# Performance work log

Hardware: AMD Instinct MI355X
Metric: run time of the kernel (lower is better)

Reference implementation:

```python
import jax, jax.numpy as jnp
import numpy as np

N, E, F_IN, H = 50000, 800000, 500, 96

def setup_inputs() -> dict:
    key = jax.random.key(0)
    ks = jax.random.split(key, 10)
    x = jax.random.normal(ks[0], (N, F_IN), dtype=jnp.float32)
    src = jax.random.randint(ks[1], (E,), 0, N, dtype=jnp.int32)
    dst = jax.random.randint(ks[2], (E,), 0, N, dtype=jnp.int32)
    perm = jax.random.permutation(ks[3], N).astype(jnp.int32)
    W1 = jax.random.normal(ks[4], (F_IN, H), dtype=jnp.float32) / np.sqrt(F_IN)
    b1 = jnp.zeros((H,), jnp.float32)
    a1 = jnp.full((H,), 0.25, jnp.float32)  # PReLU init
    W2 = jax.random.normal(ks[5], (H, H), dtype=jnp.float32) / np.sqrt(H)
    b2 = jnp.zeros((H,), jnp.float32)
    a2 = jnp.full((H,), 0.25, jnp.float32)
    Wm = jax.random.normal(ks[6], (H, H), dtype=jnp.float32) / np.sqrt(H)
    bm = jnp.zeros((H,), jnp.float32)
    return {"x": x, "src": src, "dst": dst, "perm": perm,
            "W1": W1, "b1": b1, "a1": a1, "W2": W2, "b2": b2, "a2": a2,
            "Wm": Wm, "bm": bm}

def reference(x, src, dst, perm, W1, b1, a1, W2, b2, a2, Wm, bm):
    n = x.shape[0]
    ones = jnp.ones_like(src, dtype=x.dtype)
    deg_out = jnp.clip(jax.ops.segment_sum(ones, src, num_segments=n), 1.0)
    deg_in = jnp.clip(jax.ops.segment_sum(ones, dst, num_segments=n), 1.0)
    norm_out = (deg_out ** -0.5)[:, None]  # [N,1]
    norm_in = (deg_in ** -0.5)[:, None]

    def gconv(h, W, b, a):
        # DGL GraphConv, norm='both': D_out^-1/2 -> W -> A -> D_in^-1/2 -> +b -> PReLU
        h = (h * norm_out) @ W                                  # [N,H]
        agg = jax.ops.segment_sum(h[src], dst, num_segments=n)  # SpMM via gather/scatter
        h = agg * norm_in + b
        return jnp.where(h >= 0, h, a * h)                      # PReLU

    def encode(feat):
        h = gconv(feat, W1, b1, a1)
        return gconv(h, W2, b2, a2)

    z1 = encode(x)
    z2 = encode(x[perm])  # corrupted view: permuted node features
    z1 = z1 @ Wm + bm
    z2 = z2 @ Wm + bm
    return jnp.concatenate([z1.sum(1), z2.sum(1)], axis=0)  # [2N]
```

## Files before the change

kernel.cpp:

```cpp
#include <hip/hip_runtime.h>

#define H96 96

typedef __attribute__((ext_vector_type(8))) short bf16x8_t;
typedef __attribute__((ext_vector_type(4))) float f32x4_t;
typedef __attribute__((ext_vector_type(8))) _Float16 half8_t;

__global__ void deg_kernel(const int* __restrict__ src, const int* __restrict__ dst,
                           int* __restrict__ dout, int* __restrict__ din, int E) {
    int e = blockIdx.x * blockDim.x + threadIdx.x;
    if (e < E) {
        atomicAdd(dout + src[e], 1);
        atomicAdd(din + dst[e], 1);
    }
}

__global__ void norm_kernel(const int* __restrict__ dO, const int* __restrict__ dI,
                            float* __restrict__ no, float* __restrict__ ni, int N) {
    int i = blockIdx.x * blockDim.x + threadIdx.x;
    if (i < N) {
        no[i] = rsqrtf(fmaxf((float)dO[i], 1.0f));
        ni[i] = rsqrtf(fmaxf((float)dI[i], 1.0f));
    }
}

__global__ void scanA_kernel(const int* __restrict__ in, int* __restrict__ pre,
                             int* __restrict__ bsums, int n) {
    __shared__ int s[256];
    int i = blockIdx.x * 256 + threadIdx.x;
    int v = (i < n) ? in[i] : 0;
    s[threadIdx.x] = v;
    __syncthreads();
    for (int off = 1; off < 256; off <<= 1) {
        int t = (threadIdx.x >= off) ? s[threadIdx.x - off] : 0;
        __syncthreads();
        s[threadIdx.x] += t;
        __syncthreads();
    }
    if (i < n) pre[i] = s[threadIdx.x] - v;
    if (threadIdx.x == 255) bsums[blockIdx.x] = s[255];
}

__global__ void scanB_kernel(int* __restrict__ bsums, int nb) {
    __shared__ int s[256];
    int v = (threadIdx.x < nb) ? bsums[threadIdx.x] : 0;
    s[threadIdx.x] = v;
    __syncthreads();
    for (int off = 1; off < 256; off <<= 1) {
        int t = (threadIdx.x >= off) ? s[threadIdx.x - off] : 0;
        __syncthreads();
        s[threadIdx.x] += t;
        __syncthreads();
    }
    if (threadIdx.x < nb) bsums[threadIdx.x] = s[threadIdx.x] - v;
}

__global__ void rowfin_kernel(const int* __restrict__ pre, const int* __restrict__ bsums,
                              int* __restrict__ row_start, int* __restrict__ cursor,
                              int N, int E) {
    int i = blockIdx.x * 256 + threadIdx.x;
    if (i < N) {
        int v = pre[i] + bsums[blockIdx.x];
        row_start[i] = v;
        cursor[i] = v;
    }
    if (i == 0) row_start[N] = E;
}

__global__ void scatter_kernel(const int* __restrict__ src, const int* __restrict__ dst,
                               const int* __restrict__ perm, const float* __restrict__ norm_out,
                               int* __restrict__ cursor, int4* __restrict__ edge4, int E) {
    int e = blockIdx.x * 256 + threadIdx.x;
    if (e < E) {
        int d = dst[e];
        int s = src[e];
        int p = atomicAdd(cursor + d, 1);
        edge4[p] = make_int4(s, perm[s], __float_as_int(norm_out[s]), 0);
    }
}

__global__ void histblk_kernel(const int* __restrict__ deg, int* __restrict__ hb,
                               int N, int nb) {
    __shared__ int h[256];
    h[threadIdx.x] = 0;
    __syncthreads();
    int i = blockIdx.x * 256 + threadIdx.x;
    if (i < N) atomicAdd(&h[min(deg[i], 255)], 1);
    __syncthreads();
    hb[threadIdx.x * nb + blockIdx.x] = h[threadIdx.x];
}

__global__ void place2_kernel(const int* __restrict__ deg, const int* __restrict__ hpre,
                              const int* __restrict__ bsums, int* __restrict__ order,
                              int N, int nb) {
    __shared__ int cur[256];
    int idx = threadIdx.x * nb + blockIdx.x;
    cur[threadIdx.x] = hpre[idx] + bsums[idx >> 8];
    __syncthreads();
    int i = blockIdx.x * 256 + threadIdx.x;
    if (i < N) {
        int b = min(deg[i], 255);
        int p = atomicAdd(&cur[b], 1);
        order[p] = i;
    }
}

__device__ __forceinline__ void f2bf2(float v, unsigned short& h, unsigned short& l) {
    unsigned int b = __float_as_uint(v);
    unsigned short hh = (unsigned short)((b + 0x7FFFu + ((b >> 16) & 1u)) >> 16);
    float fh = __uint_as_float(((unsigned int)hh) << 16);
    float r = v - fh;
    unsigned int rb = __float_as_uint(r);
    unsigned short ll = (unsigned short)((rb + 0x7FFFu + ((rb >> 16) & 1u)) >> 16);
    h = hh; l = ll;
}

__global__ void weights_prep(const float* __restrict__ W1, const float* __restrict__ W2,
                             const float* __restrict__ Wm, const float* __restrict__ bm,
                             unsigned short* __restrict__ w1h, unsigned short* __restrict__ w1l,
                             unsigned short* __restrict__ w2h, unsigned short* __restrict__ w2l,
                             float* __restrict__ wsum, float* __restrict__ bsum,
                             int F, int KP1) {
    int idx = blockIdx.x * 256 + threadIdx.x;
    int z1 = 96 * KP1, z2 = z1 + 96 * 96;
    if (idx < z1) {
        int n = idx / KP1, k = idx - n * KP1;
        float v = (k < F) ? W1[(size_t)k * 96 + n] : 0.f;
        unsigned short h, l;
        f2bf2(v, h, l);
        w1h[idx] = h; w1l[idx] = l;
    } else if (idx < z2) {
        int t = idx - z1;
        int n = t / 96, k = t - n * 96;
        float v = W2[(size_t)k * 96 + n];
        unsigned short h, l;
        f2bf2(v, h, l);
        w2h[t] = h; w2l[t] = l;
    } else if (idx < z2 + 96) {
        int c = idx - z2;
        float s = 0.f;
        for (int j = 0; j < 96; j++) s += Wm[c * 96 + j];
        wsum[c] = s;
    } else if (idx == z2 + 96) {
        float s = 0.f;
        for (int j = 0; j < 96; j++) s += bm[j];
        bsum[0] = s;
    }
}

#define GBM 128
#define GBK 32
#define ASTR2 40
__global__ __launch_bounds__(256) void gemm_mfma(const float* __restrict__ A,
                                                 const unsigned short* __restrict__ Bth,
                                                 const unsigned short* __restrict__ Btl,
                                                 _Float16* __restrict__ C16,
                                                 int M, int K, int KP) {
    __shared__ unsigned short As_hi[GBM * ASTR2];
    __shared__ unsigned short As_lo[GBM * ASTR2];
    __shared__ unsigned short Bs_hi[96 * ASTR2];
    __shared__ unsigned short Bs_lo[96 * ASTR2];
    int tid = threadIdx.x;
    int row0 = blockIdx.x * GBM;
    int wid = tid >> 6, lane = tid & 63;
    int q = lane >> 4, mn = lane & 15;
    f32x4_t acc[2][6] = {};
    int nk = (K + GBK - 1) / GBK;

    for (int t = 0; t < nk; t++) {
        int k0 = t * GBK;
#pragma unroll
        for (int i = 0; i < 4; i++) {
            int idx = tid + i * 256;
            int r = idx >> 3, kq = idx & 7;
            int gr = row0 + r, gk = k0 + kq * 4;
            float4 v = make_float4(0.f, 0.f, 0.f, 0.f);
            if (gr < M) {
                if (gk + 4 <= K) {
                    v = *(const float4*)(A + (size_t)gr * K + gk);
                } else {
                    float tv[4] = {0.f, 0.f, 0.f, 0.f};
                    for (int c = 0; c < 4; c++)
                        if (gk + c < K) tv[c] = A[(size_t)gr * K + gk + c];
                    v = make_float4(tv[0], tv[1], tv[2], tv[3]);
                }
            }
            unsigned short h0, l0, h1, l1, h2, l2, h3, l3;
            f2bf2(v.x, h0, l0); f2bf2(v.y, h1, l1);
            f2bf2(v.z, h2, l2); f2bf2(v.w, h3, l3);
            uint2 hv = make_uint2((unsigned)h0 | ((unsigned)h1 << 16),
                                  (unsigned)h2 | ((unsigned)h3 << 16));
            uint2 lv = make_uint2((unsigned)l0 | ((unsigned)l1 << 16),
                                  (unsigned)l2 | ((unsigned)l3 << 16));
            *(uint2*)&As_hi[r * ASTR2 + kq * 4] = hv;
            *(uint2*)&As_lo[r * ASTR2 + kq * 4] = lv;
        }
#pragma unroll
        for (int i = 0; i < 2; i++) {
            int idx = tid + i * 256;
            if (idx < 384) {
                int n = idx >> 2, kc = idx & 3;
                uint4 hv = *(const uint4*)(Bth + (size_t)n * KP + k0 + kc * 8);
                uint4 lv = *(const uint4*)(Btl + (size_t)n * KP + k0 + kc * 8);
                *(uint4*)&Bs_hi[n * ASTR2 + kc * 8] = hv;
                *(uint4*)&Bs_lo[n * ASTR2 + kc * 8] = lv;
            }
        }
        __syncthreads();

        bf16x8_t ah[2], al[2], bh[6], bl[6];
#pragma unroll
        for (int rt = 0; rt < 2; rt++) {
            int r = wid * 32 + rt * 16 + mn;
            ah[rt] = *(const bf16x8_t*)&As_hi[r * ASTR2 + q * 8];
            al[rt] = *(const bf16x8_t*)&As_lo[r * ASTR2 + q * 8];
        }
#pragma unroll
        for (int ct = 0; ct < 6; ct++) {
            int n = ct * 16 + mn;
            bh[ct] = *(const bf16x8_t*)&Bs_hi[n * ASTR2 + q * 8];
            bl[ct] = *(const bf16x8_t*)&Bs_lo[n * ASTR2 + q * 8];
        }
#pragma unroll
        for (int rt = 0; rt < 2; rt++)
#pragma unroll
            for (int ct = 0; ct < 6; ct++) {
                acc[rt][ct] = __builtin_amdgcn_mfma_f32_16x16x32_bf16(ah[rt], bh[ct], acc[rt][ct], 0, 0, 0);
                acc[rt][ct] = __builtin_amdgcn_mfma_f32_16x16x32_bf16(ah[rt], bl[ct], acc[rt][ct], 0, 0, 0);
                acc[rt][ct] = __builtin_amdgcn_mfma_f32_16x16x32_bf16(al[rt], bh[ct], acc[rt][ct], 0, 0, 0);
            }
        __syncthreads();
    }

#pragma unroll
    for (int rt = 0; rt < 2; rt++) {
#pragma unroll
        for (int reg = 0; reg < 4; reg++) {
            int gr = row0 + wid * 32 + rt * 16 + q * 4 + reg;
            if (gr < M) {
#pragma unroll
                for (int ct = 0; ct < 6; ct++)
                    C16[(size_t)gr * H96 + ct * 16 + mn] = (_Float16)acc[rt][ct][reg];
            }
        }
    }
}

__device__ __forceinline__ void fmah8(float4& a, float4& b, float s, half8_t v) {
    a.x = fmaf(s, (float)v[0], a.x); a.y = fmaf(s, (float)v[1], a.y);
    a.z = fmaf(s, (float)v[2], a.z); a.w = fmaf(s, (float)v[3], a.w);
    b.x = fmaf(s, (float)v[4], b.x); b.y = fmaf(s, (float)v[5], b.y);
    b.z = fmaf(s, (float)v[6], b.z); b.w = fmaf(s, (float)v[7], b.w);
}

__device__ __forceinline__ float4 prelu4(float4 acc, float ni, float4 b, float4 a) {
    float4 h;
    h.x = fmaf(acc.x, ni, b.x); h.x = (h.x >= 0.f) ? h.x : a.x * h.x;
    h.y = fmaf(acc.y, ni, b.y); h.y = (h.y >= 0.f) ? h.y : a.y * h.y;
    h.z = fmaf(acc.z, ni, b.z); h.z = (h.z >= 0.f) ? h.z : a.z * h.z;
    h.w = fmaf(acc.w, ni, b.w); h.w = (h.w >= 0.f) ? h.w : a.w * h.w;
    return h;
}

__global__ __launch_bounds__(384) void spmm1_dual(
        const half8_t* __restrict__ yh, const int* __restrict__ row_start,
        const int4* __restrict__ edge4, const int* __restrict__ order,
        const float* __restrict__ norm_out, const float* __restrict__ norm_in,
        const float* __restrict__ b1, const float* __restrict__ a1,
        float4* __restrict__ h1, float4* __restrict__ h2, int N) {
    int g = blockIdx.x * 32 + threadIdx.y;
    if (g >= N) return;
    int d = order[g];
    int tx = threadIdx.x;
    int beg = row_start[d], end = row_start[d + 1];
    const half8_t* yt = yh + tx;
    float4 a1a = {0,0,0,0}, a1b = {0,0,0,0}, a2a = {0,0,0,0}, a2b = {0,0,0,0};
    int j = beg;
    for (; j + 8 <= end; j += 8) {
        int4 e[8];
#pragma unroll
        for (int q = 0; q < 8; q++) e[q] = edge4[j + q];
        half8_t u[8], w[8];
#pragma unroll
        for (int q = 0; q < 8; q++) u[q] = yt[(size_t)e[q].x * 12];
#pragma unroll
        for (int q = 0; q < 8; q++) w[q] = yt[(size_t)e[q].y * 12];
#pragma unroll
        for (int q = 0; q < 8; q++) {
            float n = __int_as_float(e[q].z);
            fmah8(a1a, a1b, n, u[q]);
            fmah8(a2a, a2b, n, w[q]);
        }
    }
    for (; j < end; j++) {
        int4 e = edge4[j];
        float n = __int_as_float(e.z);
        fmah8(a1a, a1b, n, yt[(size_t)e.x * 12]);
        fmah8(a2a, a2b, n, yt[(size_t)e.y * 12]);
    }
    float ni = norm_in[d], no = norm_out[d];
    float4 bb0 = ((const float4*)b1)[tx * 2], bb1 = ((const float4*)b1)[tx * 2 + 1];
    float4 aa0 = ((const float4*)a1)[tx * 2], aa1 = ((const float4*)a1)[tx * 2 + 1];
    float4 r1a = prelu4(a1a, ni, bb0, aa0), r1b = prelu4(a1b, ni, bb1, aa1);
    float4 r2a = prelu4(a2a, ni, bb0, aa0), r2b = prelu4(a2b, ni, bb1, aa1);
    r1a.x *= no; r1a.y *= no; r1a.z *= no; r1a.w *= no;
    r1b.x *= no; r1b.y *= no; r1b.z *= no; r1b.w *= no;
    r2a.x *= no; r2a.y *= no; r2a.z *= no; r2a.w *= no;
    r2b.x *= no; r2b.y *= no; r2b.z *= no; r2b.w *= no;
    h1[(size_t)d * 24 + tx * 2] = r1a;
    h1[(size_t)d * 24 + tx * 2 + 1] = r1b;
    h2[(size_t)d * 24 + tx * 2] = r2a;
    h2[(size_t)d * 24 + tx * 2 + 1] = r2b;
}

__global__ __launch_bounds__(384) void spmm2_dual(
        const half8_t* __restrict__ th,
        const int* __restrict__ row_start, const int4* __restrict__ edge4,
        const int* __restrict__ order, const float* __restrict__ norm_in,
        const float* __restrict__ b2, const float* __restrict__ a2,
        const float* __restrict__ wsum, const float* __restrict__ bsum,
        float* __restrict__ outp, int N) {
    int g = blockIdx.x * 32 + threadIdx.y;
    int tx = threadIdx.x;
    int ty = threadIdx.y;
    bool valid = (g < N);
    int d = valid ? order[g] : 0;
    int beg = 0, end = 0;
    if (valid) { beg = row_start[d]; end = row_start[d + 1]; }
    const half8_t* t1 = th + tx;
    const half8_t* t2 = th + (size_t)N * 12 + tx;
    float4 a1a = {0,0,0,0}, a1b = {0,0,0,0}, a2a = {0,0,0,0}, a2b = {0,0,0,0};
    int j = beg;
    for (; j + 8 <= end; j += 8) {
        int s[8];
#pragma unroll
        for (int q = 0; q < 8; q++) s[q] = edge4[j + q].x;
        half8_t u[8], w[8];
#pragma unroll
        for (int q = 0; q < 8; q++) u[q] = t1[(size_t)s[q] * 12];
#pragma unroll
        for (int q = 0; q < 8; q++) w[q] = t2[(size_t)s[q] * 12];
#pragma unroll
        for (int q = 0; q < 8; q++) {
            fmah8(a1a, a1b, 1.f, u[q]);
            fmah8(a2a, a2b, 1.f, w[q]);
        }
    }
    for (; j < end; j++) {
        int s = edge4[j].x;
        fmah8(a1a, a1b, 1.f, t1[(size_t)s * 12]);
        fmah8(a2a, a2b, 1.f, t2[(size_t)s * 12]);
    }
    float ni = valid ? norm_in[d] : 0.f;
    float4 bb0 = ((const float4*)b2)[tx * 2], bb1 = ((const float4*)b2)[tx * 2 + 1];
    float4 aa0 = ((const float4*)a2)[tx * 2], aa1 = ((const float4*)a2)[tx * 2 + 1];
    float4 wv0 = ((const float4*)wsum)[tx * 2], wv1 = ((const float4*)wsum)[tx * 2 + 1];
    float4 r1a = prelu4(a1a, ni, bb0, aa0), r1b = prelu4(a1b, ni, bb1, aa1);
    float4 r2a = prelu4(a2a, ni, bb0, aa0), r2b = prelu4(a2b, ni, bb1, aa1);
    float p1 = r1a.x * wv0.x + r1a.y * wv0.y + r1a.z * wv0.z + r1a.w * wv0.w
             + r1b.x * wv1.x + r1b.y * wv1.y + r1b.z * wv1.z + r1b.w * wv1.w;
    float p2 = r2a.x * wv0.x + r2a.y * wv0.y + r2a.z * wv0.z + r2a.w * wv0.w
             + r2b.x * wv1.x + r2b.y * wv1.y + r2b.z * wv1.z + r2b.w * wv1.w;
    __shared__ float red1[32][12];
    __shared__ float red2[32][12];
    red1[ty][tx] = p1;
    red2[ty][tx] = p2;
    __syncthreads();
    if (tx == 0 && valid) {
        float s1 = 0.f, s2 = 0.f;
#pragma unroll
        for (int k = 0; k < 12; k++) { s1 += red1[ty][k]; s2 += red2[ty][k]; }
        outp[d] = s1 + bsum[0];
        outp[N + d] = s2 + bsum[0];
    }
}

extern "C" void kernel_launch(void* const* d_in, const int* in_sizes, int n_in,
                              void* d_out, int out_size, void* d_ws, size_t ws_size,
                              hipStream_t stream) {
    const float* x    = (const float*)d_in[0];
    const int*   src  = (const int*)d_in[1];
    const int*   dst  = (const int*)d_in[2];
    const int*   perm = (const int*)d_in[3];
    const float* W1   = (const float*)d_in[4];
    const float* b1   = (const float*)d_in[5];
    const float* a1   = (const float*)d_in[6];
    const float* W2   = (const float*)d_in[7];
    const float* b2   = (const float*)d_in[8];
    const float* a2   = (const float*)d_in[9];
    const float* Wm   = (const float*)d_in[10];
    const float* bm   = (const float*)d_in[11];
    float* out = (float*)d_out;

    int E = in_sizes[1];
    int N = in_sizes[3];
    int F = in_sizes[0] / N;
    int KP1 = ((F + GBK - 1) / GBK) * GBK;

    size_t NP = ((size_t)N + 256) & ~(size_t)255;
    size_t EP = ((size_t)E + 255) & ~(size_t)255;
    int nb = (N + 255) / 256;
    size_t HB = ((size_t)256 * nb + 255) & ~(size_t)255;

    int* deg_out   = (int*)d_ws;
    int* deg_in    = deg_out + NP;
    int* pre       = deg_in + NP;
    int* row_start = pre + NP;
    int* cursor    = row_start + NP;
    int* order     = cursor + NP;
    int* bsums     = order + NP;
    int* hb        = bsums + 256;
    int* hpre      = hb + HB;
    int4* edge4    = (int4*)(hpre + HB);
    float* norm_out = (float*)(edge4 + EP);
    float* norm_in  = norm_out + NP;
    float* wsum     = norm_in + NP;
    float* bsum     = wsum + 128;
    unsigned short* w1th = (unsigned short*)(bsum + 128);
    unsigned short* w1tl = w1th + 49664;
    unsigned short* w2th = w1tl + 49664;
    unsigned short* w2tl = w2th + 9728;
    _Float16* yh = (_Float16*)(w2tl + 9728);
    _Float16* th = yh + ((size_t)N * H96 + 256);
    float* h1s = (float*)(th + (size_t)2 * N * H96 + 256);

    hipMemsetAsync(deg_out, 0, 2 * NP * sizeof(int), stream);
    deg_kernel<<<(E + 255) / 256, 256, 0, stream>>>(src, dst, deg_out, deg_in, E);
    norm_kernel<<<(N + 255) / 256, 256, 0, stream>>>(deg_out, deg_in, norm_out, norm_in, N);

    scanA_kernel<<<nb, 256, 0, stream>>>(deg_in, pre, bsums, N);
    scanB_kernel<<<1, 256, 0, stream>>>(bsums, nb);
    rowfin_kernel<<<nb, 256, 0, stream>>>(pre, bsums, row_start, cursor, N, E);
    scatter_kernel<<<(E + 255) / 256, 256, 0, stream>>>(src, dst, perm, norm_out, cursor,
                                                        edge4, E);

    histblk_kernel<<<nb, 256, 0, stream>>>(deg_in, hb, N, nb);
    int n2 = 256 * nb;
    int nb2 = (n2 + 255) / 256;
    scanA_kernel<<<nb2, 256, 0, stream>>>(hb, hpre, bsums, n2);
    scanB_kernel<<<1, 256, 0, stream>>>(bsums, nb2);
    place2_kernel<<<nb, 256, 0, stream>>>(deg_in, hpre, bsums, order, N, nb);

    int wtot = 96 * KP1 + 96 * 96 + 96 + 1;
    weights_prep<<<(wtot + 255) / 256, 256, 0, stream>>>(W1, W2, Wm, bm, w1th, w1tl,
                                                         w2th, w2tl, wsum, bsum, F, KP1);

    gemm_mfma<<<(N + GBM - 1) / GBM, 256, 0, stream>>>(x, w1th, w1tl, yh, N, F, KP1);

    int nsb = (N + 31) / 32;
    spmm1_dual<<<nsb, dim3(12, 32), 0, stream>>>(
        (const half8_t*)yh, row_start, edge4, order, norm_out, norm_in,
        b1, a1, (float4*)h1s, (float4*)(h1s + (size_t)N * H96), N);

    gemm_mfma<<<(2 * N + GBM - 1) / GBM, 256, 0, stream>>>(h1s, w2th, w2tl, th, 2 * N, H96, H96);

    spmm2_dual<<<nsb, dim3(12, 32), 0, stream>>>(
        (const half8_t*)th, row_start, edge4, order, norm_in, b2, a2,
        wsum, bsum, out, N);
}
```

Before: 469.9 us.

## Prefetch GEMM tiles into registers, shrink tile, and store layer-1 output as fp16

The MFMA GEMM now loads the next K-tile of A and B into registers while the current tile is being computed, giving a simple software pipeline. The row tile drops from 128 to 64, which doubles the number of blocks. spmm1 now writes its intermediate activations as fp16 instead of fp32, and the second GEMM reads them through a new half-precision load path. Together these cut global traffic for the intermediate and hide load latency. The cost is extra rounding of the intermediate to fp16 and less reuse of B per block.

```diff
diff --git a/kernel.cpp b/kernel.cpp
--- a/kernel.cpp
+++ b/kernel.cpp
@@ -148,14 +148,14 @@
     }
 }
 
-#define GBM 128
+#define GBM 64
 #define GBK 32
 #define ASTR2 40
-__global__ __launch_bounds__(256) void gemm_mfma(const float* __restrict__ A,
+__global__ __launch_bounds__(256) void gemm_mfma(const void* __restrict__ Av,
                                                  const unsigned short* __restrict__ Bth,
                                                  const unsigned short* __restrict__ Btl,
                                                  _Float16* __restrict__ C16,
-                                                 int M, int K, int KP) {
+                                                 int M, int K, int KP, int a_half) {
     __shared__ unsigned short As_hi[GBM * ASTR2];
     __shared__ unsigned short As_lo[GBM * ASTR2];
     __shared__ unsigned short Bs_hi[96 * ASTR2];
@@ -164,86 +164,130 @@
     int row0 = blockIdx.x * GBM;
     int wid = tid >> 6, lane = tid & 63;
     int q = lane >> 4, mn = lane & 15;
-    f32x4_t acc[2][6] = {};
+    f32x4_t acc[6] = {};
     int nk = (K + GBK - 1) / GBK;
 
+    const float* A32 = (const float*)Av;
+    const _Float16* A16 = (const _Float16*)Av;
+
+    float4 pa32[2];
+    uint4 pa16 = make_uint4(0, 0, 0, 0);
+    uint4 pbh[2], pbl[2];
+
+#define LOAD_A(K0)                                                                   \
+    if (a_half) {                                                                    \
+        int r = tid >> 2, kq = tid & 3;                                              \
+        int gr = row0 + r, gk = (K0) + kq * 8;                                       \
+        pa16 = (gr < M) ? *(const uint4*)(A16 + (size_t)gr * K + gk)                 \
+                        : make_uint4(0, 0, 0, 0);                                    \
+    } else {                                                                         \
+        _Pragma("unroll")                                                            \
+        for (int i = 0; i < 2; i++) {                                                \
+            int idx = tid + i * 256;                                                 \
+            int r = idx >> 3, kq = idx & 7;                                          \
+            int gr = row0 + r, gk = (K0) + kq * 4;                                   \
+            float4 v = make_float4(0.f, 0.f, 0.f, 0.f);                              \
+            if (gr < M) {                                                            \
+                if (gk + 4 <= K) v = *(const float4*)(A32 + (size_t)gr * K + gk);    \
+                else {                                                               \
+                    float tv[4] = {0.f, 0.f, 0.f, 0.f};                              \
+                    for (int c = 0; c < 4; c++)                                      \
+                        if (gk + c < K) tv[c] = A32[(size_t)gr * K + gk + c];        \
+                    v = make_float4(tv[0], tv[1], tv[2], tv[3]);                     \
+                }                                                                    \
+            }                                                                        \
+            pa32[i] = v;                                                             \
+        }                                                                            \
+    }
+
+#define LOAD_B(K0)                                                                   \
+    _Pragma("unroll")                                                                \
+    for (int i = 0; i < 2; i++) {                                                    \
+        int idx = tid + i * 256;                                                     \
+        if (idx < 384) {                                                             \
+            int n = idx >> 2, kc = idx & 3;                                          \
+            pbh[i] = *(const uint4*)(Bth + (size_t)n * KP + (K0) + kc * 8);          \
+            pbl[i] = *(const uint4*)(Btl + (size_t)n * KP + (K0) + kc * 8);          \
+        }                                                                            \
+    }
+
+    LOAD_A(0)
+    LOAD_B(0)
+
     for (int t = 0; t < nk; t++) {
-        int k0 = t * GBK;
-#pragma unroll
-        for (int i = 0; i < 4; i++) {
-            int idx = tid + i * 256;
-            int r = idx >> 3, kq = idx & 7;
-            int gr = row0 + r, gk = k0 + kq * 4;
-            float4 v = make_float4(0.f, 0.f, 0.f, 0.f);
-            if (gr < M) {
-                if (gk + 4 <= K) {
-                    v = *(const float4*)(A + (size_t)gr * K + gk);
-                } else {
-                    float tv[4] = {0.f, 0.f, 0.f, 0.f};
-                    for (int c = 0; c < 4; c++)
-                        if (gk + c < K) tv[c] = A[(size_t)gr * K + gk + c];
-                    v = make_float4(tv[0], tv[1], tv[2], tv[3]);
-                }
+        if (a_half) {
+            int r = tid >> 2, kq = tid & 3;
+            const _Float16* hp = (const _Float16*)&pa16;
+            unsigned short hs[8], ls[8];
+#pragma unroll
+            for (int c = 0; c < 8; c++) f2bf2((float)hp[c], hs[c], ls[c]);
+            uint4 hv, lv;
+            hv.x = hs[0] | ((unsigned)hs[1] << 16); hv.y = hs[2] | ((unsigned)hs[3] << 16);
+            hv.z = hs[4] | ((unsigned)hs[5] << 16); hv.w = hs[6] | ((unsigned)hs[7] << 16);
+            lv.x = ls[0] | ((unsigned)ls[1] << 16); lv.y = ls[2] | ((unsigned)ls[3] << 16);
+            lv.z = ls[4] | ((unsigned)ls[5] << 16); lv.w = ls[6] | ((unsigned)ls[7] << 16);
+            *(uint4*)&As_hi[r * ASTR2 + kq * 8] = hv;
+            *(uint4*)&As_lo[r * ASTR2 + kq * 8] = lv;
+        } else {
+#pragma unroll
+            for (int i = 0; i < 2; i++) {
+                int idx = tid + i * 256;
+                int r = idx >> 3, kq = idx & 7;
+                float4 v = pa32[i];
+                unsigned short h0, l0, h1, l1, h2, l2, h3, l3;
+                f2bf2(v.x, h0, l0); f2bf2(v.y, h1, l1);
+                f2bf2(v.z, h2, l2); f2bf2(v.w, h3, l3);
+                uint2 hv = make_uint2((unsigned)h0 | ((unsigned)h1 << 16),
+                                      (unsigned)h2 | ((unsigned)h3 << 16));
+                uint2 lv = make_uint2((unsigned)l0 | ((unsigned)l1 << 16),
+                                      (unsigned)l2 | ((unsigned)l3 << 16));
+                *(uint2*)&As_hi[r * ASTR2 + kq * 4] = hv;
+                *(uint2*)&As_lo[r * ASTR2 + kq * 4] = lv;
             }
-            unsigned short h0, l0, h1, l1, h2, l2, h3, l3;
-            f2bf2(v.x, h0, l0); f2bf2(v.y, h1, l1);
-            f2bf2(v.z, h2, l2); f2bf2(v.w, h3, l3);
-            uint2 hv = make_uint2((unsigned)h0 | ((unsigned)h1 << 16),
-                                  (unsigned)h2 | ((unsigned)h3 << 16));
-            uint2 lv = make_uint2((unsigned)l0 | ((unsigned)l1 << 16),
-                                  (unsigned)l2 | ((unsigned)l3 << 16));
-            *(uint2*)&As_hi[r * ASTR2 + kq * 4] = hv;
-            *(uint2*)&As_lo[r * ASTR2 + kq * 4] = lv;
         }
 #pragma unroll
         for (int i = 0; i < 2; i++) {
             int idx = tid + i * 256;
             if (idx < 384) {
                 int n = idx >> 2, kc = idx & 3;
-                uint4 hv = *(const uint4*)(Bth + (size_t)n * KP + k0 + kc * 8);
-                uint4 lv = *(const uint4*)(Btl + (size_t)n * KP + k0 + kc * 8);
-                *(uint4*)&Bs_hi[n * ASTR2 + kc * 8] = hv;
-                *(uint4*)&Bs_lo[n * ASTR2 + kc * 8] = lv;
+                *(uint4*)&Bs_hi[n * ASTR2 + kc * 8] = pbh[i];
+                *(uint4*)&Bs_lo[n * ASTR2 + kc * 8] = pbl[i];
             }
         }
         __syncthreads();
 
-        bf16x8_t ah[2], al[2], bh[6], bl[6];
-#pragma unroll
-        for (int rt = 0; rt < 2; rt++) {
-            int r = wid * 32 + rt * 16 + mn;
-            ah[rt] = *(const bf16x8_t*)&As_hi[r * ASTR2 + q * 8];
-            al[rt] = *(const bf16x8_t*)&As_lo[r * ASTR2 + q * 8];
-        }
+        if (t + 1 < nk) {
+            int k0 = (t + 1) * GBK;
+            LOAD_A(k0)
+            LOAD_B(k0)
+        }
+
+        int wr = wid * 16 + mn;
+        bf16x8_t ah = *(const bf16x8_t*)&As_hi[wr * ASTR2 + q * 8];
+        bf16x8_t al = *(const bf16x8_t*)&As_lo[wr * ASTR2 + q * 8];
 #pragma unroll
         for (int ct = 0; ct < 6; ct++) {
             int n = ct * 16 + mn;
-            bh[ct] = *(const bf16x8_t*)&Bs_hi[n * ASTR2 + q * 8];
-            bl[ct] = *(const bf16x8_t*)&Bs_lo[n * ASTR2 + q * 8];
-        }
-#pragma unroll
-        for (int rt = 0; rt < 2; rt++)
-#pragma unroll
-            for (int ct = 0; ct < 6; ct++) {
-                acc[rt][ct] = __builtin_amdgcn_mfma_f32_16x16x32_bf16(ah[rt], bh[ct], acc[rt][ct], 0, 0, 0);
-                acc[rt][ct] = __builtin_amdgcn_mfma_f32_16x16x32_bf16(ah[rt], bl[ct], acc[rt][ct], 0, 0, 0);
-                acc[rt][ct] = __builtin_amdgcn_mfma_f32_16x16x32_bf16(al[rt], bh[ct], acc[rt][ct], 0, 0, 0);
-            }
+            bf16x8_t bh = *(const bf16x8_t*)&Bs_hi[n * ASTR2 + q * 8];
+            bf16x8_t bl = *(const bf16x8_t*)&Bs_lo[n * ASTR2 + q * 8];
+            acc[ct] = __builtin_amdgcn_mfma_f32_16x16x32_bf16(ah, bh, acc[ct], 0, 0, 0);
+            acc[ct] = __builtin_amdgcn_mfma_f32_16x16x32_bf16(ah, bl, acc[ct], 0, 0, 0);
+            acc[ct] = __builtin_amdgcn_mfma_f32_16x16x32_bf16(al, bh, acc[ct], 0, 0, 0);
+        }
         __syncthreads();
     }
 
 #pragma unroll
-    for (int rt = 0; rt < 2; rt++) {
-#pragma unroll
-        for (int reg = 0; reg < 4; reg++) {
-            int gr = row0 + wid * 32 + rt * 16 + q * 4 + reg;
-            if (gr < M) {
-#pragma unroll
-                for (int ct = 0; ct < 6; ct++)
-                    C16[(size_t)gr * H96 + ct * 16 + mn] = (_Float16)acc[rt][ct][reg];
-            }
-        }
-    }
+    for (int reg = 0; reg < 4; reg++) {
+        int gr = row0 + wid * 16 + q * 4 + reg;
+        if (gr < M) {
+#pragma unroll
+            for (int ct = 0; ct < 6; ct++)
+                C16[(size_t)gr * H96 + ct * 16 + mn] = (_Float16)acc[ct][reg];
+        }
+    }
+#undef LOAD_A
+#undef LOAD_B
 }
 
 __device__ __forceinline__ void fmah8(float4& a, float4& b, float s, half8_t v) {
@@ -267,7 +311,7 @@
         const int4* __restrict__ edge4, const int* __restrict__ order,
         const float* __restrict__ norm_out, const float* __restrict__ norm_in,
         const float* __restrict__ b1, const float* __restrict__ a1,
-        float4* __restrict__ h1, float4* __restrict__ h2, int N) {
+        half8_t* __restrict__ h1, half8_t* __restrict__ h2, int N) {
     int g = blockIdx.x * 32 + threadIdx.y;
     if (g >= N) return;
     int d = order[g];
@@ -303,14 +347,17 @@
     float4 aa0 = ((const float4*)a1)[tx * 2], aa1 = ((const float4*)a1)[tx * 2 + 1];
     float4 r1a = prelu4(a1a, ni, bb0, aa0), r1b = prelu4(a1b, ni, bb1, aa1);
     float4 r2a = prelu4(a2a, ni, bb0, aa0), r2b = prelu4(a2b, ni, bb1, aa1);
-    r1a.x *= no; r1a.y *= no; r1a.z *= no; r1a.w *= no;
-    r1b.x *= no; r1b.y *= no; r1b.z *= no; r1b.w *= no;
-    r2a.x *= no; r2a.y *= no; r2a.z *= no; r2a.w *= no;
-    r2b.x *= no; r2b.y *= no; r2b.z *= no; r2b.w *= no;
-    h1[(size_t)d * 24 + tx * 2] = r1a;
-    h1[(size_t)d * 24 + tx * 2 + 1] = r1b;
-    h2[(size_t)d * 24 + tx * 2] = r2a;
-    h2[(size_t)d * 24 + tx * 2 + 1] = r2b;
+    half8_t o1, o2;
+    o1[0] = (_Float16)(r1a.x * no); o1[1] = (_Float16)(r1a.y * no);
+    o1[2] = (_Float16)(r1a.z * no); o1[3] = (_Float16)(r1a.w * no);
+    o1[4] = (_Float16)(r1b.x * no); o1[5] = (_Float16)(r1b.y * no);
+    o1[6] = (_Float16)(r1b.z * no); o1[7] = (_Float16)(r1b.w * no);
+    o2[0] = (_Float16)(r2a.x * no); o2[1] = (_Float16)(r2a.y * no);
+    o2[2] = (_Float16)(r2a.z * no); o2[3] = (_Float16)(r2a.w * no);
+    o2[4] = (_Float16)(r2b.x * no); o2[5] = (_Float16)(r2b.y * no);
+    o2[6] = (_Float16)(r2b.z * no); o2[7] = (_Float16)(r2b.w * no);
+    h1[(size_t)d * 12 + tx] = o1;
+    h2[(size_t)d * 12 + tx] = o2;
 }
 
 __global__ __launch_bounds__(384) void spmm2_dual(
@@ -420,9 +467,9 @@
     unsigned short* w1tl = w1th + 49664;
     unsigned short* w2th = w1tl + 49664;
     unsigned short* w2tl = w2th + 9728;
-    _Float16* yh = (_Float16*)(w2tl + 9728);
-    _Float16* th = yh + ((size_t)N * H96 + 256);
-    float* h1s = (float*)(th + (size_t)2 * N * H96 + 256);
+    _Float16* yh  = (_Float16*)(w2tl + 9728);
+    _Float16* h1h = yh + ((size_t)N * H96 + 256);
+    _Float16* th  = h1h + ((size_t)2 * N * H96 + 256);
 
     hipMemsetAsync(deg_out, 0, 2 * NP * sizeof(int), stream);
     deg_kernel<<<(E + 255) / 256, 256, 0, stream>>>(src, dst, deg_out, deg_in, E);
@@ -445,14 +492,14 @@
     weights_prep<<<(wtot + 255) / 256, 256, 0, stream>>>(W1, W2, Wm, bm, w1th, w1tl,
                                                          w2th, w2tl, wsum, bsum, F, KP1);
 
-    gemm_mfma<<<(N + GBM - 1) / GBM, 256, 0, stream>>>(x, w1th, w1tl, yh, N, F, KP1);
+    gemm_mfma<<<(N + GBM - 1) / GBM, 256, 0, stream>>>(x, w1th, w1tl, yh, N, F, KP1, 0);
 
     int nsb = (N + 31) / 32;
     spmm1_dual<<<nsb, dim3(12, 32), 0, stream>>>(
         (const half8_t*)yh, row_start, edge4, order, norm_out, norm_in,
-        b1, a1, (float4*)h1s, (float4*)(h1s + (size_t)N * H96), N);
-
-    gemm_mfma<<<(2 * N + GBM - 1) / GBM, 256, 0, stream>>>(h1s, w2th, w2tl, th, 2 * N, H96, H96);
+        b1, a1, (half8_t*)h1h, (half8_t*)(h1h + (size_t)N * H96), N);
+
+    gemm_mfma<<<(2 * N + GBM - 1) / GBM, 256, 0, stream>>>(h1h, w2th, w2tl, th, 2 * N, H96, H96, 1);
 
     spmm2_dual<<<nsb, dim3(12, 32), 0, stream>>>(
         (const half8_t*)th, row_start, edge4, order, norm_in, b2, a2,
```

Result: slower. 502.9 us (+7.0%).
